# Kernel optimization log

Hardware: AMD Instinct MI355X
Metric: run time of the kernel (lower is better)

Reference implementation:

```python
import jax, jax.numpy as jnp
import numpy as np

N, B, CIN = 2048, 16, 1
M = 4096
COUT = 64
R = 128


def setup_inputs() -> dict:
    key = jax.random.key(0)
    k1, k2, k3, k4, k5 = jax.random.split(key, 5)
    return {
        "context_in": jax.random.normal(k1, (N, B, CIN), dtype=jnp.float32),
        "context_out": jax.random.normal(k2, (N, B, COUT), dtype=jnp.float32),
        "target_in": jax.random.normal(k3, (M, B, CIN), dtype=jnp.float32),
        "lengthscale": jnp.ones((1,), dtype=jnp.float32),
        "W": jax.random.normal(k4, (R, COUT + 1), dtype=jnp.float32),
        "b": jax.random.normal(k5, (R,), dtype=jnp.float32),
    }


def reference(context_in, context_out, target_in, lengthscale, W, b):
    # context_in: (N,B,Cin), context_out: (N,B,Cout), target_in: (M,B,Cin)
    n, batch, _ = context_in.shape
    # density channel prepended -> (N,B,Cout+1)
    dens = jnp.ones((n, batch, 1), dtype=context_in.dtype)
    co = jnp.concatenate([dens, context_out], axis=-1)
    ci = jnp.transpose(context_in, (1, 0, 2))   # (B,N,Cin)
    ti = jnp.transpose(target_in, (1, 0, 2))    # (B,M,Cin)
    # squared pairwise distances (B,N,M)
    d2 = (jnp.sum(ci * ci, -1)[:, :, None]
          + jnp.sum(ti * ti, -1)[:, None, :]
          - 2.0 * jnp.einsum('bnd,bmd->bnm', ci, ti))
    d2 = jnp.maximum(d2, 0.0)
    # RBF kernel: exp(-0.5 * d2 / lengthscale^2)
    K = jnp.exp(-0.5 * d2 / (lengthscale[0] ** 2))  # (B,N,M)
    # weighted sum over context points: (B,M,Cout+1)
    out = jnp.einsum('nbc,bnm->bmc', co, K)
    # density normalization of non-density channels
    out = jnp.concatenate([out[..., :1], out[..., 1:] / (out[..., :1] + 1e-8)], axis=-1)
    # linear projection (Cout+1 -> R)
    out = out @ W.T + b
    return jnp.transpose(out, (1, 0, 2))  # (M,B,R)
```

## Files before the change

kernel.cpp:

```cpp
#include <hip/hip_runtime.h>
#include <hip/hip_bf16.h>


#define N_CTX 2048
#define BATCH 16
#define M_TGT 4096
#define COUT  64
#define RDIM  128

#define WS_CO_BYTES (N_CTX * BATCH * COUT * 2)
#define WS_SX_OFF   WS_CO_BYTES
#define WS_WT_OFF   (WS_SX_OFF + N_CTX * BATCH * 4)

#define SSCALE 0.8493222f

typedef __attribute__((ext_vector_type(8)))  short        bf16x8;
typedef __attribute__((ext_vector_type(4)))  float        floatx4;
typedef __attribute__((ext_vector_type(4)))  unsigned int uint4v;

#if __has_builtin(__builtin_amdgcn_exp2f)
#define EXP2F __builtin_amdgcn_exp2f
#else
#define EXP2F exp2f
#endif

static __device__ __forceinline__ unsigned int pack_bf16(float lo, float hi) {
    __hip_bfloat162 h = __float22bfloat162_rn(make_float2(lo, hi));
    return *reinterpret_cast<unsigned int*>(&h);
}
static __device__ __forceinline__ unsigned short f2bf(float f) {
    __hip_bfloat16 h = __float2bfloat16(f);
    return *reinterpret_cast<unsigned short*>(&h);
}

__global__ __launch_bounds__(256)
void convdeepset_prep(const float* __restrict__ ci, const float* __restrict__ co,
                      const float* __restrict__ ls, const float* __restrict__ W,
                      unsigned char* __restrict__ ws)
{
    unsigned short* cow = (unsigned short*)ws;
    float*          sx  = (float*)(ws + WS_SX_OFF);
    unsigned short* wt  = (unsigned short*)(ws + WS_WT_OFF);
    const int blk = blockIdx.x, tid = threadIdx.x;

    if (blk < 1024) {
        const int g    = blk * 4 + (tid >> 6);
        const int bb   = g & 15;
        const int nblk = g >> 4;
        const int c    = tid & 63;
        const float* rp = co + ((size_t)nblk * 8 * BATCH + bb) * COUT + c;
        unsigned int u[4];
#pragma unroll
        for (int j = 0; j < 4; ++j) {
            const float f0 = rp[(size_t)(2 * j)     * BATCH * COUT];
            const float f1 = rp[(size_t)(2 * j + 1) * BATCH * COUT];
            u[j] = pack_bf16(f0, f1);
        }
        *(uint4v*)&cow[(size_t)bb * 131072 + nblk * 512 + c * 8] = *(uint4v*)u;
    } else if (blk < 1152) {
        const int f = (blk - 1024) * 256 + tid;
        const int n = f & 2047, bb = f >> 11;
        const float s = SSCALE / ls[0];
        sx[bb * 2048 + n] = s * ci[(size_t)n * BATCH + bb];
    } else {
        for (int f = tid; f < 8192; f += 256) {
            const int cp = f & 7, r = (f >> 3) & 127, ch = f >> 10;
            wt[ch * 1024 + r * 8 + cp] = f2bf(W[r * 65 + 1 + ch * 8 + cp]);
        }
    }
}

__global__ __launch_bounds__(256, 7)
void convdeepset_main(const float* __restrict__ ti, const float* __restrict__ ls,
                      const float* __restrict__ W,  const float* __restrict__ bias,
                      const unsigned char* __restrict__ ws, float* __restrict__ out)
{
    __shared__ float sxt[N_CTX];
    __shared__ unsigned int rbuf[2 * 64 * 12];
    __shared__ unsigned short vstage[2][1024];
    __shared__ float w0l[RDIM], biasl[RDIM];

    const int tid  = threadIdx.x;
    const int lane = tid & 63;
    const int wv   = tid >> 6;
    const int mh   = wv & 1;
    const int nh   = wv >> 1;
    const int g2   = lane >> 4;
    const int l15  = lane & 15;

    const int xcd = blockIdx.x & 7;
    const int i   = blockIdx.x >> 3;
    const int b   = xcd * 2 + (i & 1);
    const int mt  = i >> 1;
    const int m0  = mt * 32 + mh * 16;

    const float4* sxg = (const float4*)(ws + WS_SX_OFF) + b * (N_CTX / 4);
    float4* s4 = (float4*)sxt;
    s4[tid]       = sxg[tid];
    s4[tid + 256] = sxg[tid + 256];
    if (tid < RDIM) { w0l[tid] = W[tid * 65]; biasl[tid] = bias[tid]; }

    const float s  = SSCALE / ls[0];
    const float sy = s * ti[(size_t)(m0 + l15) * BATCH + b];
    __syncthreads();

    const short onebf = (short)0x3F80;
    bf16x8 ones;
#pragma unroll
    for (int j = 0; j < 8; ++j) ones[j] = onebf;

    const int ks0 = nh * 32;
    const unsigned short* cowB = (const unsigned short*)ws
                               + (size_t)b * 131072 + (ks0 * 4 + g2) * 512 + l15 * 8;

    floatx4 acc[4], accd;
#pragma unroll
    for (int q = 0; q < 4; ++q)
#pragma unroll
        for (int e = 0; e < 4; ++e) acc[q][e] = 0.0f;
#pragma unroll
    for (int e = 0; e < 4; ++e) accd[e] = 0.0f;

#pragma unroll 2
    for (int ks = 0; ks < 32; ++ks) {
        const unsigned short* p = cowB + (size_t)ks * 2048;
        const bf16x8 c0 = *(const bf16x8*)(p);
        const bf16x8 c1 = *(const bf16x8*)(p + 128);
        const bf16x8 c2 = *(const bf16x8*)(p + 256);
        const bf16x8 c3 = *(const bf16x8*)(p + 384);
        const float* xp = &sxt[(ks0 + ks) * 32 + g2 * 8];
        const float4 xa = *(const float4*)(xp);
        const float4 xb = *(const float4*)(xp + 4);
        float kv[8];
        {
            float t;
            t = xa.x - sy; kv[0] = EXP2F(-(t * t));
            t = xa.y - sy; kv[1] = EXP2F(-(t * t));
            t = xa.z - sy; kv[2] = EXP2F(-(t * t));
            t = xa.w - sy; kv[3] = EXP2F(-(t * t));
            t = xb.x - sy; kv[4] = EXP2F(-(t * t));
            t = xb.y - sy; kv[5] = EXP2F(-(t * t));
            t = xb.z - sy; kv[6] = EXP2F(-(t * t));
            t = xb.w - sy; kv[7] = EXP2F(-(t * t));
        }
        uint4v aw;
#pragma unroll
        for (int q2 = 0; q2 < 4; ++q2) aw[q2] = pack_bf16(kv[2 * q2], kv[2 * q2 + 1]);
        const bf16x8 av = __builtin_bit_cast(bf16x8, aw);
        acc[0] = __builtin_amdgcn_mfma_f32_16x16x32_bf16(av, c0, acc[0], 0, 0, 0);
        acc[1] = __builtin_amdgcn_mfma_f32_16x16x32_bf16(av, c1, acc[1], 0, 0, 0);
        acc[2] = __builtin_amdgcn_mfma_f32_16x16x32_bf16(av, c2, acc[2], 0, 0, 0);
        acc[3] = __builtin_amdgcn_mfma_f32_16x16x32_bf16(av, c3, acc[3], 0, 0, 0);
        accd   = __builtin_amdgcn_mfma_f32_16x16x32_bf16(av, ones, accd, 0, 0, 0);
    }

    if (nh == 1) {
        unsigned int* slot = &rbuf[(mh * 64 + lane) * 12];
        unsigned int pu[8];
#pragma unroll
        for (int reg = 0; reg < 4; ++reg)
#pragma unroll
            for (int qp = 0; qp < 2; ++qp)
                pu[reg * 2 + qp] = pack_bf16(acc[2 * qp][reg], acc[2 * qp + 1][reg]);
        *(uint4v*)(slot)     = *(uint4v*)(pu);
        *(uint4v*)(slot + 4) = *(uint4v*)(pu + 4);
        *(uint4v*)(slot + 8) = __builtin_bit_cast(uint4v, accd);
    }
    __syncthreads();
    if (nh == 1) return;

    {
        const unsigned int* slot = &rbuf[(mh * 64 + lane) * 12];
        const uint4v r0 = *(const uint4v*)(slot);
        const uint4v r1 = *(const uint4v*)(slot + 4);
        const floatx4 rd = __builtin_bit_cast(floatx4, *(const uint4v*)(slot + 8));
#pragma unroll
        for (int reg = 0; reg < 4; ++reg)
#pragma unroll
            for (int qp = 0; qp < 2; ++qp) {
                const int j = reg * 2 + qp;
                const unsigned int u = (j < 4) ? r0[j] : r1[j - 4];
                acc[2 * qp][reg]     += __builtin_bit_cast(float, u << 16);
                acc[2 * qp + 1][reg] += __builtin_bit_cast(float, u & 0xffff0000u);
            }
#pragma unroll
        for (int e = 0; e < 4; ++e) accd[e] += rd[e];
    }

    float drow[4], dinv[4];
#pragma unroll
    for (int reg = 0; reg < 4; ++reg) {
        drow[reg] = accd[reg];
        dinv[reg] = 1.0f / (accd[reg] + 1e-8f);
    }

    unsigned short* vs = vstage[mh];
#pragma unroll
    for (int reg = 0; reg < 4; ++reg) {
        const int m = (lane >> 4) * 4 + reg;
#pragma unroll
        for (int q = 0; q < 4; ++q) {
            const int c = q * 16 + l15;
            vs[(c >> 3) * 128 + m * 8 + (c & 7)] = f2bf(acc[q][reg]);
        }
    }

    const unsigned short* wtg = (const unsigned short*)(ws + WS_WT_OFF);
    floatx4 pacc[8];
#pragma unroll
    for (int rt = 0; rt < 8; ++rt)
#pragma unroll
        for (int e = 0; e < 4; ++e) pacc[rt][e] = 0.0f;

#pragma unroll
    for (int s2 = 0; s2 < 2; ++s2) {
        const int ch = s2 * 4 + g2;
        const bf16x8 avp = *(const bf16x8*)&vs[ch * 128 + l15 * 8];
#pragma unroll
        for (int rt = 0; rt < 8; ++rt) {
            const bf16x8 bvp = *(const bf16x8*)&wtg[ch * 1024 + (rt * 16 + l15) * 8];
            pacc[rt] = __builtin_amdgcn_mfma_f32_16x16x32_bf16(avp, bvp, pacc[rt], 0, 0, 0);
        }
    }

#pragma unroll
    for (int rt = 0; rt < 8; ++rt) {
        const int r = rt * 16 + l15;
        const float w0v = w0l[r];
        const float bv  = biasl[r];
#pragma unroll
        for (int reg = 0; reg < 4; ++reg) {
            const int m = (lane >> 4) * 4 + reg;
            out[((size_t)(m0 + m) * BATCH + b) * RDIM + r]
                = pacc[rt][reg] * dinv[reg] + drow[reg] * w0v + bv;
        }
    }
}

extern "C" void kernel_launch(void* const* d_in, const int* in_sizes, int n_in,
                              void* d_out, int out_size, void* d_ws, size_t ws_size,
                              hipStream_t stream) {
    const float* ci   = (const float*)d_in[0];
    const float* co   = (const float*)d_in[1];
    const float* ti   = (const float*)d_in[2];
    const float* ls   = (const float*)d_in[3];
    const float* W    = (const float*)d_in[4];
    const float* bias = (const float*)d_in[5];
    float* o = (float*)d_out;
    (void)in_sizes; (void)n_in; (void)out_size; (void)ws_size;

    convdeepset_prep<<<1153, 256, 0, stream>>>(ci, co, ls, W, (unsigned char*)d_ws);
    convdeepset_main<<<2048, 256, 0, stream>>>(
        ti, ls, W, bias, (const unsigned char*)d_ws, o);
}
```

Baseline: 123.6 us.

## Stage context tiles in LDS via async loads and widen per-wave M tile

Restructures the main kernel so each block covers 128 targets and each wave covers 32 targets across the full context range, which removes the split-K reduction through shared memory. Context-output tiles are double-buffered in LDS using global_load_lds async copies and shared by all four waves, where before each wave read them directly from global memory. The grid shrinks from 2048 to 512 blocks, and each wave keeps two sets of accumulators. The intent is to raise data reuse and reduce global traffic, at the cost of fewer blocks, higher register and LDS use, and a barrier in every period.

```diff
diff --git a/kernel.cpp b/kernel.cpp
--- a/kernel.cpp
+++ b/kernel.cpp
@@ -70,21 +70,19 @@
     }
 }
 
-__global__ __launch_bounds__(256, 7)
+__global__ __launch_bounds__(256)
 void convdeepset_main(const float* __restrict__ ti, const float* __restrict__ ls,
                       const float* __restrict__ W,  const float* __restrict__ bias,
                       const unsigned char* __restrict__ ws, float* __restrict__ out)
 {
     __shared__ float sxt[N_CTX];
-    __shared__ unsigned int rbuf[2 * 64 * 12];
-    __shared__ unsigned short vstage[2][1024];
+    __shared__ unsigned short slab[2][8192];
+    __shared__ unsigned short vstage[4][2][1024];
     __shared__ float w0l[RDIM], biasl[RDIM];
 
     const int tid  = threadIdx.x;
     const int lane = tid & 63;
     const int wv   = tid >> 6;
-    const int mh   = wv & 1;
-    const int nh   = wv >> 1;
     const int g2   = lane >> 4;
     const int l15  = lane & 15;
 
@@ -92,147 +90,138 @@
     const int i   = blockIdx.x >> 3;
     const int b   = xcd * 2 + (i & 1);
     const int mt  = i >> 1;
-    const int m0  = mt * 32 + mh * 16;
+    const int m0  = mt * 128 + wv * 32;
 
     const float4* sxg = (const float4*)(ws + WS_SX_OFF) + b * (N_CTX / 4);
-    float4* s4 = (float4*)sxt;
-    s4[tid]       = sxg[tid];
-    s4[tid + 256] = sxg[tid + 256];
+    ((float4*)sxt)[tid]       = sxg[tid];
+    ((float4*)sxt)[tid + 256] = sxg[tid + 256];
     if (tid < RDIM) { w0l[tid] = W[tid * 65]; biasl[tid] = bias[tid]; }
 
-    const float s  = SSCALE / ls[0];
-    const float sy = s * ti[(size_t)(m0 + l15) * BATCH + b];
-    __syncthreads();
+    const float s   = SSCALE / ls[0];
+    const float sy0 = s * ti[(size_t)(m0 + l15) * BATCH + b];
+    const float sy1 = s * ti[(size_t)(m0 + 16 + l15) * BATCH + b];
+
+    const unsigned short* cowb = (const unsigned short*)ws + (size_t)b * 131072;
+
+    typedef const __attribute__((address_space(1))) unsigned int* gp_t;
+    typedef __attribute__((address_space(3))) unsigned int* lp_t;
+    auto stage = [&](int period, int buf) {
+        const unsigned short* gsrc = cowb + (size_t)period * 8192;
+#pragma unroll
+        for (int j = 0; j < 4; ++j) {
+            const int ch = wv * 4 + j;
+            __builtin_amdgcn_global_load_lds((gp_t)(gsrc + ch * 512 + lane * 8),
+                                             (lp_t)(&slab[buf][ch * 512]),
+                                             16, 0, 0);
+        }
+    };
 
     const short onebf = (short)0x3F80;
     bf16x8 ones;
 #pragma unroll
     for (int j = 0; j < 8; ++j) ones[j] = onebf;
 
-    const int ks0 = nh * 32;
-    const unsigned short* cowB = (const unsigned short*)ws
-                               + (size_t)b * 131072 + (ks0 * 4 + g2) * 512 + l15 * 8;
-
-    floatx4 acc[4], accd;
+    floatx4 acc0[4], acc1[4], accd0, accd1;
 #pragma unroll
     for (int q = 0; q < 4; ++q)
 #pragma unroll
-        for (int e = 0; e < 4; ++e) acc[q][e] = 0.0f;
-#pragma unroll
-    for (int e = 0; e < 4; ++e) accd[e] = 0.0f;
-
-#pragma unroll 2
-    for (int ks = 0; ks < 32; ++ks) {
-        const unsigned short* p = cowB + (size_t)ks * 2048;
-        const bf16x8 c0 = *(const bf16x8*)(p);
-        const bf16x8 c1 = *(const bf16x8*)(p + 128);
-        const bf16x8 c2 = *(const bf16x8*)(p + 256);
-        const bf16x8 c3 = *(const bf16x8*)(p + 384);
-        const float* xp = &sxt[(ks0 + ks) * 32 + g2 * 8];
-        const float4 xa = *(const float4*)(xp);
-        const float4 xb = *(const float4*)(xp + 4);
-        float kv[8];
-        {
-            float t;
-            t = xa.x - sy; kv[0] = EXP2F(-(t * t));
-            t = xa.y - sy; kv[1] = EXP2F(-(t * t));
-            t = xa.z - sy; kv[2] = EXP2F(-(t * t));
-            t = xa.w - sy; kv[3] = EXP2F(-(t * t));
-            t = xb.x - sy; kv[4] = EXP2F(-(t * t));
-            t = xb.y - sy; kv[5] = EXP2F(-(t * t));
-            t = xb.z - sy; kv[6] = EXP2F(-(t * t));
-            t = xb.w - sy; kv[7] = EXP2F(-(t * t));
-        }
-        uint4v aw;
-#pragma unroll
-        for (int q2 = 0; q2 < 4; ++q2) aw[q2] = pack_bf16(kv[2 * q2], kv[2 * q2 + 1]);
-        const bf16x8 av = __builtin_bit_cast(bf16x8, aw);
-        acc[0] = __builtin_amdgcn_mfma_f32_16x16x32_bf16(av, c0, acc[0], 0, 0, 0);
-        acc[1] = __builtin_amdgcn_mfma_f32_16x16x32_bf16(av, c1, acc[1], 0, 0, 0);
-        acc[2] = __builtin_amdgcn_mfma_f32_16x16x32_bf16(av, c2, acc[2], 0, 0, 0);
-        acc[3] = __builtin_amdgcn_mfma_f32_16x16x32_bf16(av, c3, acc[3], 0, 0, 0);
-        accd   = __builtin_amdgcn_mfma_f32_16x16x32_bf16(av, ones, accd, 0, 0, 0);
+        for (int e = 0; e < 4; ++e) { acc0[q][e] = 0.0f; acc1[q][e] = 0.0f; }
+#pragma unroll
+    for (int e = 0; e < 4; ++e) { accd0[e] = 0.0f; accd1[e] = 0.0f; }
+
+    stage(0, 0);
+    __syncthreads();
+
+    for (int p = 0; p < 16; ++p) {
+        if (p + 1 < 16) stage(p + 1, (p + 1) & 1);
+        const unsigned short* sb = &slab[p & 1][0];
+#pragma unroll
+        for (int k2 = 0; k2 < 4; ++k2) {
+            const int ks = p * 4 + k2;
+            const float* xp = &sxt[ks * 32 + g2 * 8];
+            const float4 xa = *(const float4*)(xp);
+            const float4 xb = *(const float4*)(xp + 4);
+            const unsigned short* bp = sb + (k2 * 4 + g2) * 512 + l15 * 8;
+            const bf16x8 c0 = *(const bf16x8*)(bp);
+            const bf16x8 c1 = *(const bf16x8*)(bp + 128);
+            const bf16x8 c2 = *(const bf16x8*)(bp + 256);
+            const bf16x8 c3 = *(const bf16x8*)(bp + 384);
+            const float xs[8] = {xa.x, xa.y, xa.z, xa.w, xb.x, xb.y, xb.z, xb.w};
+            float kv0[8], kv1[8];
+#pragma unroll
+            for (int j = 0; j < 8; ++j) {
+                float t0 = xs[j] - sy0; kv0[j] = EXP2F(-(t0 * t0));
+                float t1 = xs[j] - sy1; kv1[j] = EXP2F(-(t1 * t1));
+            }
+            uint4v aw0, aw1;
+#pragma unroll
+            for (int q = 0; q < 4; ++q) {
+                aw0[q] = pack_bf16(kv0[2 * q], kv0[2 * q + 1]);
+                aw1[q] = pack_bf16(kv1[2 * q], kv1[2 * q + 1]);
+            }
+            const bf16x8 av0 = __builtin_bit_cast(bf16x8, aw0);
+            const bf16x8 av1 = __builtin_bit_cast(bf16x8, aw1);
+            acc0[0] = __builtin_amdgcn_mfma_f32_16x16x32_bf16(av0, c0, acc0[0], 0, 0, 0);
+            acc0[1] = __builtin_amdgcn_mfma_f32_16x16x32_bf16(av0, c1, acc0[1], 0, 0, 0);
+            acc0[2] = __builtin_amdgcn_mfma_f32_16x16x32_bf16(av0, c2, acc0[2], 0, 0, 0);
+            acc0[3] = __builtin_amdgcn_mfma_f32_16x16x32_bf16(av0, c3, acc0[3], 0, 0, 0);
+            accd0   = __builtin_amdgcn_mfma_f32_16x16x32_bf16(av0, ones, accd0, 0, 0, 0);
+            acc1[0] = __builtin_amdgcn_mfma_f32_16x16x32_bf16(av1, c0, acc1[0], 0, 0, 0);
+            acc1[1] = __builtin_amdgcn_mfma_f32_16x16x32_bf16(av1, c1, acc1[1], 0, 0, 0);
+            acc1[2] = __builtin_amdgcn_mfma_f32_16x16x32_bf16(av1, c2, acc1[2], 0, 0, 0);
+            acc1[3] = __builtin_amdgcn_mfma_f32_16x16x32_bf16(av1, c3, acc1[3], 0, 0, 0);
+            accd1   = __builtin_amdgcn_mfma_f32_16x16x32_bf16(av1, ones, accd1, 0, 0, 0);
+        }
+        __syncthreads();
     }
 
-    if (nh == 1) {
-        unsigned int* slot = &rbuf[(mh * 64 + lane) * 12];
-        unsigned int pu[8];
-#pragma unroll
-        for (int reg = 0; reg < 4; ++reg)
-#pragma unroll
-            for (int qp = 0; qp < 2; ++qp)
-                pu[reg * 2 + qp] = pack_bf16(acc[2 * qp][reg], acc[2 * qp + 1][reg]);
-        *(uint4v*)(slot)     = *(uint4v*)(pu);
-        *(uint4v*)(slot + 4) = *(uint4v*)(pu + 4);
-        *(uint4v*)(slot + 8) = __builtin_bit_cast(uint4v, accd);
-    }
-    __syncthreads();
-    if (nh == 1) return;
-
-    {
-        const unsigned int* slot = &rbuf[(mh * 64 + lane) * 12];
-        const uint4v r0 = *(const uint4v*)(slot);
-        const uint4v r1 = *(const uint4v*)(slot + 4);
-        const floatx4 rd = __builtin_bit_cast(floatx4, *(const uint4v*)(slot + 8));
-#pragma unroll
-        for (int reg = 0; reg < 4; ++reg)
-#pragma unroll
-            for (int qp = 0; qp < 2; ++qp) {
-                const int j = reg * 2 + qp;
-                const unsigned int u = (j < 4) ? r0[j] : r1[j - 4];
-                acc[2 * qp][reg]     += __builtin_bit_cast(float, u << 16);
-                acc[2 * qp + 1][reg] += __builtin_bit_cast(float, u & 0xffff0000u);
-            }
-#pragma unroll
-        for (int e = 0; e < 4; ++e) accd[e] += rd[e];
-    }
-
-    float drow[4], dinv[4];
-#pragma unroll
-    for (int reg = 0; reg < 4; ++reg) {
-        drow[reg] = accd[reg];
-        dinv[reg] = 1.0f / (accd[reg] + 1e-8f);
-    }
-
-    unsigned short* vs = vstage[mh];
-#pragma unroll
-    for (int reg = 0; reg < 4; ++reg) {
-        const int m = (lane >> 4) * 4 + reg;
-#pragma unroll
-        for (int q = 0; q < 4; ++q) {
-            const int c = q * 16 + l15;
-            vs[(c >> 3) * 128 + m * 8 + (c & 7)] = f2bf(acc[q][reg]);
-        }
-    }
-
     const unsigned short* wtg = (const unsigned short*)(ws + WS_WT_OFF);
-    floatx4 pacc[8];
-#pragma unroll
-    for (int rt = 0; rt < 8; ++rt)
-#pragma unroll
-        for (int e = 0; e < 4; ++e) pacc[rt][e] = 0.0f;
-
-#pragma unroll
-    for (int s2 = 0; s2 < 2; ++s2) {
-        const int ch = s2 * 4 + g2;
-        const bf16x8 avp = *(const bf16x8*)&vs[ch * 128 + l15 * 8];
-#pragma unroll
-        for (int rt = 0; rt < 8; ++rt) {
-            const bf16x8 bvp = *(const bf16x8*)&wtg[ch * 1024 + (rt * 16 + l15) * 8];
-            pacc[rt] = __builtin_amdgcn_mfma_f32_16x16x32_bf16(avp, bvp, pacc[rt], 0, 0, 0);
-        }
-    }
-
-#pragma unroll
-    for (int rt = 0; rt < 8; ++rt) {
-        const int r = rt * 16 + l15;
-        const float w0v = w0l[r];
-        const float bv  = biasl[r];
+#pragma unroll
+    for (int tile = 0; tile < 2; ++tile) {
+        const floatx4* acc  = tile ? acc1 : acc0;
+        const floatx4  accd = tile ? accd1 : accd0;
+        float drow[4], dinv[4];
+#pragma unroll
+        for (int e = 0; e < 4; ++e) {
+            drow[e] = accd[e];
+            dinv[e] = 1.0f / (accd[e] + 1e-8f);
+        }
+        unsigned short* vs = vstage[wv][tile];
 #pragma unroll
         for (int reg = 0; reg < 4; ++reg) {
             const int m = (lane >> 4) * 4 + reg;
-            out[((size_t)(m0 + m) * BATCH + b) * RDIM + r]
-                = pacc[rt][reg] * dinv[reg] + drow[reg] * w0v + bv;
+#pragma unroll
+            for (int q = 0; q < 4; ++q) {
+                const int c = q * 16 + l15;
+                vs[(c >> 3) * 128 + m * 8 + (c & 7)] = f2bf(acc[q][reg]);
+            }
+        }
+        floatx4 pacc[8];
+#pragma unroll
+        for (int rt = 0; rt < 8; ++rt)
+#pragma unroll
+            for (int e = 0; e < 4; ++e) pacc[rt][e] = 0.0f;
+#pragma unroll
+        for (int s2 = 0; s2 < 2; ++s2) {
+            const int ch = s2 * 4 + g2;
+            const bf16x8 avp = *(const bf16x8*)&vs[ch * 128 + l15 * 8];
+#pragma unroll
+            for (int rt = 0; rt < 8; ++rt) {
+                const bf16x8 bvp = *(const bf16x8*)&wtg[ch * 1024 + (rt * 16 + l15) * 8];
+                pacc[rt] = __builtin_amdgcn_mfma_f32_16x16x32_bf16(avp, bvp, pacc[rt], 0, 0, 0);
+            }
+        }
+#pragma unroll
+        for (int rt = 0; rt < 8; ++rt) {
+            const int r = rt * 16 + l15;
+            const float w0v = w0l[r];
+            const float bv  = biasl[r];
+#pragma unroll
+            for (int reg = 0; reg < 4; ++reg) {
+                const int m = (lane >> 4) * 4 + reg;
+                out[((size_t)(m0 + tile * 16 + m) * BATCH + b) * RDIM + r]
+                    = pacc[rt][reg] * dinv[reg] + drow[reg] * w0v + bv;
+            }
         }
     }
 }
@@ -250,6 +239,6 @@
     (void)in_sizes; (void)n_in; (void)out_size; (void)ws_size;
 
     convdeepset_prep<<<1153, 256, 0, stream>>>(ci, co, ls, W, (unsigned char*)d_ws);
-    convdeepset_main<<<2048, 256, 0, stream>>>(
+    convdeepset_main<<<512, 256, 0, stream>>>(
         ti, ls, W, bias, (const unsigned char*)d_ws, o);
 }
```

Result: no change. 122.0 us (-1.3%).
